# Performance work log

Measured on AMD Instinct MI355X. Metric: run time of the kernel, lower is better.

## Reference

```python
import jax, jax.numpy as jnp
import numpy as np

B, NQ, HW, D, H = 4, 100, 4096, 1024, 16
HD = D // H  # head dim = 64
EPS = 1e-5
NEG = -1e9


def layernorm(x, g, b):
    mu = jnp.mean(x, axis=-1, keepdims=True)
    var = jnp.mean(jnp.square(x - mu), axis=-1, keepdims=True)
    return (x - mu) * jax.lax.rsqrt(var + EPS) * g + b


def setup_inputs() -> dict:
    key = jax.random.key(0)
    ks = jax.random.split(key, 6)
    scale = 0.02
    return {
        "q": jax.random.normal(ks[0], (B, NQ, D), dtype=jnp.float32),
        "kv": jax.random.normal(ks[1], (B, HW, D), dtype=jnp.float32),
        "mask": jax.random.randint(ks[2], (B, NQ, HW), 0, 2, dtype=jnp.int32),
        "in_proj_w": scale * jax.random.normal(ks[3], (3 * D, D), dtype=jnp.float32),
        "in_proj_b": jnp.zeros((3 * D,), dtype=jnp.float32),
        "out_w": scale * jax.random.normal(ks[4], (D, D), dtype=jnp.float32),
        "out_b": jnp.zeros((D,), dtype=jnp.float32),
        "g_q": jnp.ones((D,), dtype=jnp.float32),
        "b_q": jnp.zeros((D,), dtype=jnp.float32),
        "g_kv": jnp.ones((D,), dtype=jnp.float32),
        "b_kv": jnp.zeros((D,), dtype=jnp.float32),
    }


def reference(q, kv, mask, in_proj_w, in_proj_b, out_w, out_b, g_q, b_q, g_kv, b_kv):
    qn = layernorm(q, g_q, b_q)      # [B,NQ,D]
    kvn = layernorm(kv, g_kv, b_kv)  # [B,HW,D]

    # nn.MultiheadAttention fused in-projection: rows [Wq; Wk; Wv]
    Wq, Wk, Wv = jnp.split(in_proj_w, 3, axis=0)
    bq, bk, bv = jnp.split(in_proj_b, 3, axis=0)
    qp = (qn @ Wq.T + bq).reshape(B, NQ, H, HD)
    kp = (kvn @ Wk.T + bk).reshape(B, HW, H, HD)
    vp = (kvn @ Wv.T + bv).reshape(B, HW, H, HD)

    scores = jnp.einsum("bqhd,bkhd->bhqk", qp, kp) / jnp.sqrt(jnp.float32(HD))

    # Per-query key mask; a query with an all-zero mask attends everywhere
    # (original code sets key_padding_mask=None when kpm.all()).
    allowed = mask.astype(bool)                                   # [B,NQ,HW]
    has_any = jnp.any(allowed, axis=-1, keepdims=True)
    eff = jnp.where(has_any, allowed, True)
    scores = jnp.where(eff[:, None, :, :], scores, NEG)

    attn = jax.nn.softmax(scores, axis=-1)                        # [B,H,NQ,HW]
    ctx = jnp.einsum("bhqk,bkhd->bqhd", attn, vp).reshape(B, NQ, D)
    return ctx @ out_w.T + out_b
```

## Files before the change

kernel.cpp:

```cpp
#include <hip/hip_runtime.h>
#include <math.h>
#include <stdint.h>

#define B_    4
#define NQ_   100
#define HW_   4096
#define D_    1024
#define H_    16
#define HD_   64
#define NCH_  8
#define KCH_  (HW_/NCH_)
#define QT_   32
#define MP_   512

typedef __attribute__((ext_vector_type(8))) short short8;
typedef __attribute__((ext_vector_type(8))) unsigned short ushort8v;
typedef __attribute__((ext_vector_type(4))) float f32x4;

__device__ __forceinline__ unsigned short f2bf(float f) {
    unsigned int u = __float_as_uint(f);
    u += 0x7fffu + ((u >> 16) & 1u);
    return (unsigned short)(u >> 16);
}
__device__ __forceinline__ float bf2f(unsigned short h) {
    return __uint_as_float(((unsigned int)h) << 16);
}

__device__ __forceinline__ void gl2lds16(const void* g, void* l) {
    typedef __attribute__((address_space(1))) unsigned int gu32;
    typedef __attribute__((address_space(3))) unsigned int lu32;
    __builtin_amdgcn_global_load_lds(
        reinterpret_cast<gu32*>(reinterpret_cast<uintptr_t>(g)),
        reinterpret_cast<lu32*>(reinterpret_cast<uintptr_t>(l)),
        16, 0, 0);
}

__global__ __launch_bounds__(256) void ln_bf16_kernel(
    const float* __restrict__ x, const float* __restrict__ g,
    const float* __restrict__ be, unsigned short* __restrict__ y, int real_rows)
{
    const int wv = threadIdx.x >> 6, lane = threadIdx.x & 63;
    const int row = blockIdx.x * 4 + wv;
    unsigned short* yr = y + (size_t)row * D_;
    if (row >= real_rows) {
        #pragma unroll
        for (int k = 0; k < 4; ++k)
            *reinterpret_cast<ushort4*>(yr + lane*4 + k*256) = make_ushort4(0,0,0,0);
        return;
    }
    const float* xr = x + (size_t)row * D_;
    float4 v[4];
    float s = 0.f, ss = 0.f;
    #pragma unroll
    for (int k = 0; k < 4; ++k) {
        v[k] = *reinterpret_cast<const float4*>(xr + lane*4 + k*256);
        s  += v[k].x + v[k].y + v[k].z + v[k].w;
        ss += v[k].x*v[k].x + v[k].y*v[k].y + v[k].z*v[k].z + v[k].w*v[k].w;
    }
    #pragma unroll
    for (int o = 1; o < 64; o <<= 1) {
        s  += __shfl_xor(s,  o);
        ss += __shfl_xor(ss, o);
    }
    const float mu = s * (1.0f / D_);
    const float rs = rsqrtf(ss * (1.0f / D_) - mu*mu + 1e-5f);
    #pragma unroll
    for (int k = 0; k < 4; ++k) {
        const float4 gg = *reinterpret_cast<const float4*>(g  + lane*4 + k*256);
        const float4 bb = *reinterpret_cast<const float4*>(be + lane*4 + k*256);
        ushort4 o;
        o.x = f2bf((v[k].x - mu) * rs * gg.x + bb.x);
        o.y = f2bf((v[k].y - mu) * rs * gg.y + bb.y);
        o.z = f2bf((v[k].z - mu) * rs * gg.z + bb.z);
        o.w = f2bf((v[k].w - mu) * rs * gg.w + bb.w);
        *reinterpret_cast<ushort4*>(yr + lane*4 + k*256) = o;
    }
}

__global__ __launch_bounds__(256) void wconv_kernel(
    const float* __restrict__ w, unsigned short* __restrict__ wb)
{
    const int i = blockIdx.x * 256 + threadIdx.x;
    const float4 v = reinterpret_cast<const float4*>(w)[i];
    ushort4 o;
    o.x = f2bf(v.x); o.y = f2bf(v.y); o.z = f2bf(v.z); o.w = f2bf(v.w);
    reinterpret_cast<ushort4*>(wb)[i] = o;
}

__global__ __launch_bounds__(256) void hilo_a_kernel(
    const float* __restrict__ x, unsigned short* __restrict__ y)
{
    const int row = blockIdx.x;
    const int tid = threadIdx.x;
    unsigned short* yr = y + (size_t)row * 3072;
    if (row >= B_*NQ_) {
        const ushort4 z = make_ushort4(0,0,0,0);
        reinterpret_cast<ushort4*>(yr)[tid]        = z;
        reinterpret_cast<ushort4*>(yr + 1024)[tid] = z;
        reinterpret_cast<ushort4*>(yr + 2048)[tid] = z;
        return;
    }
    const float4 v = reinterpret_cast<const float4*>(x + (size_t)row * D_)[tid];
    ushort4 hi, lo;
    hi.x = f2bf(v.x); hi.y = f2bf(v.y); hi.z = f2bf(v.z); hi.w = f2bf(v.w);
    lo.x = f2bf(v.x - bf2f(hi.x)); lo.y = f2bf(v.y - bf2f(hi.y));
    lo.z = f2bf(v.z - bf2f(hi.z)); lo.w = f2bf(v.w - bf2f(hi.w));
    reinterpret_cast<ushort4*>(yr)[tid]        = hi;
    reinterpret_cast<ushort4*>(yr + 1024)[tid] = lo;
    reinterpret_cast<ushort4*>(yr + 2048)[tid] = hi;
}

__global__ __launch_bounds__(256) void hilo_w_kernel(
    const float* __restrict__ w, unsigned short* __restrict__ y)
{
    const int row = blockIdx.x;
    const int tid = threadIdx.x;
    const float4 v = reinterpret_cast<const float4*>(w + (size_t)row * D_)[tid];
    ushort4 hi, lo;
    hi.x = f2bf(v.x); hi.y = f2bf(v.y); hi.z = f2bf(v.z); hi.w = f2bf(v.w);
    lo.x = f2bf(v.x - bf2f(hi.x)); lo.y = f2bf(v.y - bf2f(hi.y));
    lo.z = f2bf(v.z - bf2f(hi.z)); lo.w = f2bf(v.w - bf2f(hi.w));
    unsigned short* yr = y + (size_t)row * 3072;
    reinterpret_cast<ushort4*>(yr)[tid]        = hi;
    reinterpret_cast<ushort4*>(yr + 1024)[tid] = hi;
    reinterpret_cast<ushort4*>(yr + 2048)[tid] = lo;
}

__global__ __launch_bounds__(256) void mpack_kernel(
    const int* __restrict__ mask, unsigned int* __restrict__ mp)
{
    const int qrow = blockIdx.x;
    const int b = blockIdx.y;
    const int tid = threadIdx.x;
    unsigned int word = 0;
    if (qrow < NQ_ && tid < 128) {
        const int4* mr = reinterpret_cast<const int4*>(
            mask + ((size_t)(b*NQ_ + qrow))*HW_ + tid*32);
        #pragma unroll
        for (int j = 0; j < 8; ++j) {
            const int4 v = mr[j];
            word |= (v.x!=0 ? 1u:0u) << (4*j);
            word |= (v.y!=0 ? 1u:0u) << (4*j+1);
            word |= (v.z!=0 ? 1u:0u) << (4*j+2);
            word |= (v.w!=0 ? 1u:0u) << (4*j+3);
        }
    }
    const int wany = __any(word != 0) ? 1 : 0;
    __shared__ int red[4];
    if ((tid & 63) == 0) red[tid >> 6] = wany;
    __syncthreads();
    const int hasany = red[0] | red[1] | red[2] | red[3];
    if (tid < 128)
        mp[((size_t)(b*128 + qrow))*128 + tid] = hasany ? word : 0xFFFFFFFFu;
}

__global__ __launch_bounds__(256) void gemm_kv_kernel(
    const unsigned short* __restrict__ A, const unsigned short* __restrict__ Wb,
    const float* __restrict__ bias, unsigned short* __restrict__ kp,
    unsigned short* __restrict__ vt)
{
    const int K = D_;
    __shared__ __align__(16) unsigned short As[4096];
    __shared__ __align__(16) unsigned short Bs[4096];

    const int tid  = threadIdx.x;
    const int wave = tid >> 6, lane = tid & 63;
    const int bn = blockIdx.x, bm = blockIdx.y;
    const int wm = (wave >> 1) * 64, wn = (wave & 1) * 64;

    const int r0  = tid >> 2;
    const int xs  = (r0 & 3) ^ ((r0 >> 2) & 3);
    const int kc  = (tid & 3) ^ xs;
    const unsigned short* ap0 = A  + (size_t)(bm*128 + r0      )*K + kc*8;
    const unsigned short* ap1 = A  + (size_t)(bm*128 + r0 + 64 )*K + kc*8;
    const unsigned short* bp0 = Wb + (size_t)(bn*128 + r0      )*K + kc*8;
    const unsigned short* bp1 = Wb + (size_t)(bn*128 + r0 + 64 )*K + kc*8;
    unsigned short* asd0 = As + wave*512;
    unsigned short* asd1 = As + 2048 + wave*512;
    unsigned short* bsd0 = Bs + wave*512;
    unsigned short* bsd1 = Bs + 2048 + wave*512;

    f32x4 acc[4][4];
    #pragma unroll
    for (int i = 0; i < 4; ++i)
        #pragma unroll
        for (int j = 0; j < 4; ++j)
            acc[i][j] = (f32x4){0.f, 0.f, 0.f, 0.f};

    const int lr = lane & 15, lq = lane >> 4;
    const int xl = (lr & 3) ^ ((lr >> 2) & 3);
    const int qs = (lq ^ xl) * 8;

    for (int kb = 0; kb < K; kb += 32) {
        gl2lds16(ap0, asd0); gl2lds16(ap1, asd1);
        gl2lds16(bp0, bsd0); gl2lds16(bp1, bsd1);
        ap0 += 32; ap1 += 32; bp0 += 32; bp1 += 32;
        __syncthreads();
        short8 af[4], bf[4];
        #pragma unroll
        for (int i = 0; i < 4; ++i) {
            af[i] = *reinterpret_cast<const short8*>(&As[(wm + i*16 + lr)*32 + qs]);
            bf[i] = *reinterpret_cast<const short8*>(&Bs[(wn + i*16 + lr)*32 + qs]);
        }
        #pragma unroll
        for (int i = 0; i < 4; ++i)
            #pragma unroll
            for (int j = 0; j < 4; ++j)
                acc[i][j] = __builtin_amdgcn_mfma_f32_16x16x32_bf16(
                    af[i], bf[j], acc[i][j], 0, 0, 0);
        __syncthreads();
    }

    const int row0 = bm*128 + wm + lq*4;
    const int col0 = bn*128 + wn + lr;
    if (bn < 8) {
        #pragma unroll
        for (int j = 0; j < 4; ++j) {
            const int n = col0 + j*16;
            const float bb = bias[n];
            #pragma unroll
            for (int i = 0; i < 4; ++i) {
                unsigned short* Cp = kp + (size_t)(row0 + i*16) * 1024 + n;
                #pragma unroll
                for (int r = 0; r < 4; ++r)
                    Cp[(size_t)r * 1024] = f2bf(acc[i][j][r] + bb);
            }
        }
    } else {
        const int b = bm >> 5;
        const int key0base = row0 - b*4096;
        #pragma unroll
        for (int j = 0; j < 4; ++j) {
            const int n = col0 + j*16;
            const float bb = bias[n];
            unsigned short* vrow = vt + (size_t)(b*1024 + n - 1024) * HW_;
            #pragma unroll
            for (int i = 0; i < 4; ++i) {
                ushort4 o;
                o.x = f2bf(acc[i][j][0] + bb);
                o.y = f2bf(acc[i][j][1] + bb);
                o.z = f2bf(acc[i][j][2] + bb);
                o.w = f2bf(acc[i][j][3] + bb);
                *reinterpret_cast<ushort4*>(vrow + key0base + i*16) = o;
            }
        }
    }
}

__global__ __launch_bounds__(256) void gemm_splitk_kernel(
    const unsigned short* __restrict__ A, const unsigned short* __restrict__ W,
    float* __restrict__ P, int K, int KS)
{
    __shared__ __align__(16) unsigned short As[2048];
    __shared__ __align__(16) unsigned short Bs[2048];
    const int tid = threadIdx.x;
    const int wave = tid >> 6, lane = tid & 63;
    const int lr = lane & 15, quad = lane >> 4;
    const int bn = blockIdx.x, bm = blockIdx.y, sk = blockIdx.z;

    const int r0 = tid >> 2;
    const int xs = (r0 & 3) ^ ((r0 >> 2) & 3);
    const int kc = (tid & 3) ^ xs;
    const unsigned short* ap = A + (size_t)(bm*64 + r0)*K + sk*KS + kc*8;
    const unsigned short* bp = W + (size_t)(bn*64 + r0)*K + sk*KS + kc*8;
    unsigned short* asd = As + wave*512;
    unsigned short* bsd = Bs + wave*512;

    f32x4 acc[4];
    #pragma unroll
    for (int j = 0; j < 4; ++j) acc[j] = (f32x4){0.f,0.f,0.f,0.f};

    const int arow = wave*16 + lr;
    const int xa = (arow & 3) ^ ((arow >> 2) & 3);
    const int aoff = (arow*4 + (quad ^ xa))*8;
    int boff[4];
    #pragma unroll
    for (int j = 0; j < 4; ++j) {
        const int brow = j*16 + lr;
        const int xb = (brow & 3) ^ ((brow >> 2) & 3);
        boff[j] = (brow*4 + (quad ^ xb))*8;
    }

    const int nsteps = KS >> 5;
    for (int s = 0; s < nsteps; ++s) {
        gl2lds16(ap, asd); gl2lds16(bp, bsd);
        ap += 32; bp += 32;
        __syncthreads();
        const short8 af = *reinterpret_cast<const short8*>(&As[aoff]);
        short8 bf[4];
        #pragma unroll
        for (int j = 0; j < 4; ++j)
            bf[j] = *reinterpret_cast<const short8*>(&Bs[boff[j]]);
        #pragma unroll
        for (int j = 0; j < 4; ++j)
            acc[j] = __builtin_amdgcn_mfma_f32_16x16x32_bf16(af, bf[j], acc[j], 0, 0, 0);
        __syncthreads();
    }

    float* Pb = P + ((size_t)sk*MP_ + bm*64)*1024 + bn*64;
    const int m0 = wave*16 + quad*4;
    #pragma unroll
    for (int j = 0; j < 4; ++j)
        #pragma unroll
        for (int r = 0; r < 4; ++r)
            Pb[(size_t)(m0 + r)*1024 + j*16 + lr] = acc[j][r];
}

__global__ __launch_bounds__(256) void reduce_kernel(
    const float* __restrict__ P, const float* __restrict__ bias,
    float* __restrict__ Cout, int SK)
{
    const int i4 = blockIdx.x * 256 + threadIdx.x;
    const int c4 = i4 & 255;
    float4 s = reinterpret_cast<const float4*>(bias)[c4];
    for (int sk = 0; sk < SK; ++sk) {
        const float4 p = reinterpret_cast<const float4*>(P + (size_t)sk*MP_*1024)[i4];
        s.x += p.x; s.y += p.y; s.z += p.z; s.w += p.w;
    }
    reinterpret_cast<float4*>(Cout)[i4] = s;
}

__global__ __launch_bounds__(256) void flash_kernel(
    const float* __restrict__ qp, const unsigned short* __restrict__ kp,
    const unsigned short* __restrict__ vt, const unsigned int* __restrict__ mpack,
    float* __restrict__ partO, float* __restrict__ partL)
{
    __shared__ __align__(16) unsigned char smem[49152];
    unsigned short* Ks  = (unsigned short*)smem;
    unsigned short* Vts = (unsigned short*)(smem + 16384);
    unsigned short* Qs  = (unsigned short*)(smem + 32768);
    unsigned short* Ps  = (unsigned short*)(smem + 37376);
    unsigned int*   MWs = (unsigned int*)  (smem + 47616);
    float*          mlW = (float*)         (smem + 48128);
    float*          Om  = (float*)smem;

    const int tid = threadIdx.x;
    const int wave = tid >> 6, lane = tid & 63;
    const int lr = lane & 15, quad = lane >> 4;
    const int qt = blockIdx.x, h = blockIdx.y;
    const int b = blockIdx.z >> 3, ks = blockIdx.z & 7;
    const int kb0 = ks * KCH_;

    {
        const int q = tid >> 3, dc = (tid & 7) * 8;
        const int qg = qt*QT_ + q;
        float4 v0 = make_float4(0.f,0.f,0.f,0.f), v1 = v0;
        if (qg < NQ_) {
            const float* src = qp + ((size_t)(b*NQ_ + qg))*D_ + h*HD_ + dc;
            v0 = *reinterpret_cast<const float4*>(src);
            v1 = *reinterpret_cast<const float4*>(src + 4);
        }
        ushort8v o;
        o[0]=f2bf(v0.x*0.125f); o[1]=f2bf(v0.y*0.125f);
        o[2]=f2bf(v0.z*0.125f); o[3]=f2bf(v0.w*0.125f);
        o[4]=f2bf(v1.x*0.125f); o[5]=f2bf(v1.y*0.125f);
        o[6]=f2bf(v1.z*0.125f); o[7]=f2bf(v1.w*0.125f);
        *reinterpret_cast<ushort8v*>(&Qs[q*72 + dc]) = o;
    }

    const unsigned short* kptr[4];
    const unsigned short* vptr[4];
    #pragma unroll
    for (int i = 0; i < 4; ++i) {
        const int s = i*256 + tid;
        const int key = s >> 3, jg = (s & 7) ^ (key & 7);
        kptr[i] = kp + ((size_t)(b*HW_) + kb0 + key)*1024 + h*HD_ + jg*8;
        const int d = s >> 4, js = s & 15, jg2 = js ^ (d & 15);
        vptr[i] = vt + ((size_t)(b*1024 + h*HD_ + d))*HW_ + kb0 + jg2*8;
    }

    int koff[2][2], voff[4];
    #pragma unroll
    for (int kj = 0; kj < 2; ++kj)
        #pragma unroll
        for (int ds = 0; ds < 2; ++ds) {
            const int key_l = wave*32 + kj*16 + lr;
            const int jg = ds*4 + quad;
            koff[kj][ds] = (key_l*8 + (jg ^ (key_l & 7))) * 8;
        }
    #pragma unroll
    for (int dj = 0; dj < 4; ++dj) {
        const int d_l = dj*16 + lr;
        const int jg = wave*4 + quad;
        voff[dj] = (d_l*16 + (jg ^ (d_l & 15))) * 8;
    }

    float lreg[8];
    #pragma unroll
    for (int i = 0; i < 8; ++i) lreg[i] = 0.f;
    f32x4 Ov[2][4];
    #pragma unroll
    for (int i = 0; i < 2; ++i)
        #pragma unroll
        for (int j = 0; j < 4; ++j)
            Ov[i][j] = (f32x4){0.f,0.f,0.f,0.f};

    for (int kt = 0; kt < 4; ++kt) {
        __syncthreads();
        #pragma unroll
        for (int i = 0; i < 4; ++i) {
            gl2lds16(kptr[i], Ks  + (i*256 + wave*64)*8);
            gl2lds16(vptr[i], Vts + (i*256 + wave*64)*8);
            kptr[i] += 128*1024; vptr[i] += 128;
        }
        if (tid < 128) {
            const int mw = tid >> 5, mq = tid & 31;
            MWs[mw*32 + mq] = mpack[((size_t)(b*128 + qt*QT_ + mq))*128 +
                                    (ks*16 + kt*4 + mw)];
        }
        __syncthreads();

        f32x4 S[2][2];
        #pragma unroll
        for (int i = 0; i < 2; ++i)
            #pragma unroll
            for (int kj = 0; kj < 2; ++kj)
                S[i][kj] = (f32x4){0.f,0.f,0.f,0.f};
        #pragma unroll
        for (int ds = 0; ds < 2; ++ds) {
            short8 aq[2], bk[2];
            aq[0] = *reinterpret_cast<const short8*>(&Qs[(     lr)*72 + ds*32 + quad*8]);
            aq[1] = *reinterpret_cast<const short8*>(&Qs[(16 + lr)*72 + ds*32 + quad*8]);
            bk[0] = *reinterpret_cast<const short8*>(&Ks[koff[0][ds]]);
            bk[1] = *reinterpret_cast<const short8*>(&Ks[koff[1][ds]]);
            #pragma unroll
            for (int i = 0; i < 2; ++i)
                #pragma unroll
                for (int kj = 0; kj < 2; ++kj)
                    S[i][kj] = __builtin_amdgcn_mfma_f32_16x16x32_bf16(
                        aq[i], bk[kj], S[i][kj], 0, 0, 0);
        }

        #pragma unroll
        for (int i = 0; i < 2; ++i) {
            #pragma unroll
            for (int r = 0; r < 4; ++r) {
                const int q = i*16 + quad*4 + r;
                const unsigned int mw = MWs[wave*32 + q];
                const float p0 = ((mw >> lr) & 1u)        ? __expf(S[i][0][r]) : 0.f;
                const float p1 = ((mw >> (16 + lr)) & 1u) ? __expf(S[i][1][r]) : 0.f;
                lreg[i*4+r] += p0 + p1;
                const float p0n = __shfl_xor(p0, 1);
                const float p1n = __shfl_xor(p1, 1);
                if (!(lr & 1)) {
                    const unsigned int w0 = (unsigned)f2bf(p0) | ((unsigned)f2bf(p0n) << 16);
                    const unsigned int w1 = (unsigned)f2bf(p1) | ((unsigned)f2bf(p1n) << 16);
                    *reinterpret_cast<unsigned int*>(&Ps[wave*1280 + q*40 + lr])      = w0;
                    *reinterpret_cast<unsigned int*>(&Ps[wave*1280 + q*40 + 16 + lr]) = w1;
                }
            }
        }

        short8 pf[2], vf[4];
        #pragma unroll
        for (int i = 0; i < 2; ++i)
            pf[i] = *reinterpret_cast<const short8*>(&Ps[wave*1280 + (i*16+lr)*40 + quad*8]);
        #pragma unroll
        for (int dj = 0; dj < 4; ++dj)
            vf[dj] = *reinterpret_cast<const short8*>(&Vts[voff[dj]]);
        #pragma unroll
        for (int i = 0; i < 2; ++i)
            #pragma unroll
            for (int dj = 0; dj < 4; ++dj)
                Ov[i][dj] = __builtin_amdgcn_mfma_f32_16x16x32_bf16(
                    pf[i], vf[dj], Ov[i][dj], 0, 0, 0);
    }

    __syncthreads();
    #pragma unroll
    for (int i = 0; i < 2; ++i)
        #pragma unroll
        for (int r = 0; r < 4; ++r) {
            float l = lreg[i*4+r];
            #pragma unroll
            for (int o = 1; o < 16; o <<= 1) l += __shfl_xor(l, o);
            if (lr == 0) mlW[wave*32 + i*16 + quad*4 + r] = l;
        }
    #pragma unroll
    for (int i = 0; i < 2; ++i)
        #pragma unroll
        for (int dj = 0; dj < 4; ++dj)
            #pragma unroll
            for (int r = 0; r < 4; ++r) {
                const int q = i*16 + quad*4 + r;
                Om[wave*2112 + q*66 + dj*16 + lr] = Ov[i][dj][r];
            }
    __syncthreads();
    {
        const int q = tid >> 3, dc = (tid & 7) * 8;
        float L = 0.f;
        #pragma unroll
        for (int w = 0; w < 4; ++w) L += mlW[w*32 + q];
        float os[8] = {};
        #pragma unroll
        for (int w = 0; w < 4; ++w)
            #pragma unroll
            for (int j = 0; j < 8; ++j)
                os[j] += Om[w*2112 + q*66 + dc + j];
        const size_t pr = (((size_t)(b*H_ + h))*NCH_ + ks)*128 + qt*QT_ + q;
        *reinterpret_cast<float4*>(&partO[pr*HD_ + dc])     = make_float4(os[0],os[1],os[2],os[3]);
        *reinterpret_cast<float4*>(&partO[pr*HD_ + dc + 4]) = make_float4(os[4],os[5],os[6],os[7]);
        if ((tid & 7) == 0) partL[pr] = L;
    }
}

__global__ __launch_bounds__(64) void combine_kernel(
    const float* __restrict__ partO, const float* __restrict__ partL,
    float* __restrict__ ctx)
{
    const int d = threadIdx.x;
    const int qi = blockIdx.x, h = blockIdx.y, b = blockIdx.z;
    const size_t base = ((size_t)(b*H_ + h)) * NCH_ * 128;
    float L = 0.f, O = 0.f;
    #pragma unroll
    for (int i = 0; i < NCH_; ++i) {
        const size_t r = base + i*128 + qi;
        L += partL[r];
        O += partO[r*HD_ + d];
    }
    ctx[((size_t)(b*NQ_ + qi))*D_ + h*HD_ + d] = O / L;
}

extern "C" void kernel_launch(void* const* d_in, const int* in_sizes, int n_in,
                              void* d_out, int out_size, void* d_ws, size_t ws_size,
                              hipStream_t stream)
{
    const float* q     = (const float*)d_in[0];
    const float* kv    = (const float*)d_in[1];
    const int*   mask  = (const int*)  d_in[2];
    const float* in_w  = (const float*)d_in[3];
    const float* in_b  = (const float*)d_in[4];
    const float* out_w = (const float*)d_in[5];
    const float* out_b = (const float*)d_in[6];
    const float* g_q   = (const float*)d_in[7];
    const float* b_q   = (const float*)d_in[8];
    const float* g_kv  = (const float*)d_in[9];
    const float* b_kv  = (const float*)d_in[10];
    float* out = (float*)d_out;

    char* ws = (char*)d_ws;
    float*          qp       = (float*)         (ws + 0);
    unsigned int*   mpackp   = (unsigned int*)  (ws + 1638400);
    unsigned short* wfull_bf = (unsigned short*)(ws + 1900544);
    unsigned short* qn_bf    = (unsigned short*)(ws + 8192000);
    unsigned short* ctx_cat  = (unsigned short*)(ws + 9240576);
    unsigned short* wout_cat = (unsigned short*)(ws + 12386304);
    float*          P        = (float*)         (ws + 18677760);
    float*          ctx      = (float*)         (ws + 35454976);
    float*          partL    = (float*)         (ws + 37093376);
    float*          partO    = (float*)         (ws + 37355520);
    unsigned short* kvn_bf   = (unsigned short*)(ws + 54132736);
    unsigned short* kp       = (unsigned short*)(ws + 87687168);
    unsigned short* vt       = (unsigned short*)(ws + 121241600);

    mpack_kernel<<<dim3(128, B_), 256, 0, stream>>>(mask, mpackp);
    wconv_kernel<<<3*D_*D_/4/256, 256, 0, stream>>>(in_w, wfull_bf);
    ln_bf16_kernel<<<B_*HW_/4, 256, 0, stream>>>(kv, g_kv, b_kv, kvn_bf, B_*HW_);
    ln_bf16_kernel<<<MP_/4, 256, 0, stream>>>(q, g_q, b_q, qn_bf, B_*NQ_);

    gemm_splitk_kernel<<<dim3(D_/64, MP_/64, 8), 256, 0, stream>>>(
        qn_bf, wfull_bf, P, D_, 128);
    reduce_kernel<<<B_*NQ_*D_/4/256, 256, 0, stream>>>(P, in_b, qp, 8);

    gemm_kv_kernel<<<dim3(16, B_*HW_/128), 256, 0, stream>>>(
        kvn_bf, wfull_bf + (size_t)D_*D_, in_b + D_, kp, vt);

    flash_kernel<<<dim3(4, H_, B_*NCH_), 256, 0, stream>>>(
        qp, kp, vt, mpackp, partO, partL);
    combine_kernel<<<dim3(NQ_, H_, B_), 64, 0, stream>>>(partO, partL, ctx);

    hilo_a_kernel<<<MP_, 256, 0, stream>>>(ctx, ctx_cat);
    hilo_w_kernel<<<D_, 256, 0, stream>>>(out_w, wout_cat);
    gemm_splitk_kernel<<<dim3(D_/64, MP_/64, 8), 256, 0, stream>>>(
        ctx_cat, wout_cat, P, 3*D_, 384);
    reduce_kernel<<<B_*NQ_*D_/4/256, 256, 0, stream>>>(P, out_b, out, 8);
}
```

Baseline: 332.8 us.

## Rewrite KV projection GEMM with 256x256 tiles and 4-stage LDS pipeline

The K/V projection GEMM moves from 128x128 tiles with 256 threads and a single-buffered LDS stage to 256x256 tiles with 512 threads (8 waves, each computing a 128x64 sub-tile). Global-to-LDS loads now run through a 4-deep ring buffer using explicit vmcnt waits, barriers and raised MFMA priority, so memory traffic overlaps compute. The larger tile raises operand reuse per byte loaded. In exchange the kernel uses 128KB of dynamic LDS and many more accumulator registers, the launch grid is smaller, and the waitcnt/barrier sequencing is fragile.

Result: no change. 327.1 us (-1.7%).

```diff
diff --git a/kernel.cpp b/kernel.cpp
--- a/kernel.cpp
+++ b/kernel.cpp
@@ -34,6 +34,11 @@
         reinterpret_cast<lu32*>(reinterpret_cast<uintptr_t>(l)),
         16, 0, 0);
 }
+
+#define VMCNT8() asm volatile("s_waitcnt vmcnt(8)" ::: "memory")
+#define VMCNT0() asm volatile("s_waitcnt vmcnt(0)" ::: "memory")
+#define BARRIER() do { __builtin_amdgcn_s_barrier(); \
+                       __builtin_amdgcn_sched_barrier(0); } while (0)
 
 __global__ __launch_bounds__(256) void ln_bf16_kernel(
     const float* __restrict__ x, const float* __restrict__ g,
@@ -154,94 +159,137 @@
         mp[((size_t)(b*128 + qrow))*128 + tid] = hasany ? word : 0xFFFFFFFFu;
 }
 
-__global__ __launch_bounds__(256) void gemm_kv_kernel(
+__global__ __launch_bounds__(512, 2) void gemm_kv_kernel(
     const unsigned short* __restrict__ A, const unsigned short* __restrict__ Wb,
     const float* __restrict__ bias, unsigned short* __restrict__ kp,
     unsigned short* __restrict__ vt)
 {
-    const int K = D_;
-    __shared__ __align__(16) unsigned short As[4096];
-    __shared__ __align__(16) unsigned short Bs[4096];
+    extern __shared__ __align__(16) unsigned short lds[];
+    unsigned short* As = lds;
+    unsigned short* Bs = lds + 32768;
 
     const int tid  = threadIdx.x;
-    const int wave = tid >> 6, lane = tid & 63;
-    const int bn = blockIdx.x, bm = blockIdx.y;
-    const int wm = (wave >> 1) * 64, wn = (wave & 1) * 64;
-
-    const int r0  = tid >> 2;
-    const int xs  = (r0 & 3) ^ ((r0 >> 2) & 3);
-    const int kc  = (tid & 3) ^ xs;
-    const unsigned short* ap0 = A  + (size_t)(bm*128 + r0      )*K + kc*8;
-    const unsigned short* ap1 = A  + (size_t)(bm*128 + r0 + 64 )*K + kc*8;
-    const unsigned short* bp0 = Wb + (size_t)(bn*128 + r0      )*K + kc*8;
-    const unsigned short* bp1 = Wb + (size_t)(bn*128 + r0 + 64 )*K + kc*8;
-    unsigned short* asd0 = As + wave*512;
-    unsigned short* asd1 = As + 2048 + wave*512;
-    unsigned short* bsd0 = Bs + wave*512;
-    unsigned short* bsd1 = Bs + 2048 + wave*512;
-
-    f32x4 acc[4][4];
-    #pragma unroll
-    for (int i = 0; i < 4; ++i)
+    const int wave = tid >> 6;
+    const int lane = tid & 63;
+    const int lr   = lane & 15, quad = lane >> 4;
+    const int wm2  = wave >> 2;
+    const int wn4  = wave & 3;
+
+    const int bn = blockIdx.x & 7;
+    const int bm = blockIdx.x >> 3;
+
+    const int swz_src = ((lane >> 2) & 3) ^ (lane >> 4);
+    const int scol    = ((lane & 3) ^ swz_src) * 8;
+    const unsigned short* aSrc0 = A  + (size_t)(bm*256 +       wave*16 + (lane>>2))*D_ + scol;
+    const unsigned short* aSrc1 = A  + (size_t)(bm*256 + 128 + wave*16 + (lane>>2))*D_ + scol;
+    const unsigned short* bSrc0 = Wb + (size_t)(bn*256 +       wave*16 + (lane>>2))*D_ + scol;
+    const unsigned short* bSrc1 = Wb + (size_t)(bn*256 + 128 + wave*16 + (lane>>2))*D_ + scol;
+    const int wdst = wave * 512;
+
+    const int kq = (quad ^ (lr & 3) ^ (lr >> 2)) * 8;
+    int aoff[8], boff[4];
+    #pragma unroll
+    for (int fm = 0; fm < 8; ++fm) aoff[fm] = (wm2*128 + fm*16 + lr)*32 + kq;
+    #pragma unroll
+    for (int fn = 0; fn < 4; ++fn) boff[fn] = (wn4*64  + fn*16 + lr)*32 + kq;
+
+    f32x4 acc[8][4];
+    #pragma unroll
+    for (int i = 0; i < 8; ++i)
         #pragma unroll
         for (int j = 0; j < 4; ++j)
             acc[i][j] = (f32x4){0.f, 0.f, 0.f, 0.f};
 
-    const int lr = lane & 15, lq = lane >> 4;
-    const int xl = (lr & 3) ^ ((lr >> 2) & 3);
-    const int qs = (lq ^ xl) * 8;
-
-    for (int kb = 0; kb < K; kb += 32) {
-        gl2lds16(ap0, asd0); gl2lds16(ap1, asd1);
-        gl2lds16(bp0, bsd0); gl2lds16(bp1, bsd1);
-        ap0 += 32; ap1 += 32; bp0 += 32; bp1 += 32;
-        __syncthreads();
-        short8 af[4], bf[4];
-        #pragma unroll
-        for (int i = 0; i < 4; ++i) {
-            af[i] = *reinterpret_cast<const short8*>(&As[(wm + i*16 + lr)*32 + qs]);
-            bf[i] = *reinterpret_cast<const short8*>(&Bs[(wn + i*16 + lr)*32 + qs]);
-        }
-        #pragma unroll
-        for (int i = 0; i < 4; ++i)
-            #pragma unroll
-            for (int j = 0; j < 4; ++j)
-                acc[i][j] = __builtin_amdgcn_mfma_f32_16x16x32_bf16(
-                    af[i], bf[j], acc[i][j], 0, 0, 0);
-        __syncthreads();
-    }
-
-    const int row0 = bm*128 + wm + lq*4;
-    const int col0 = bn*128 + wn + lr;
-    if (bn < 8) {
-        #pragma unroll
-        for (int j = 0; j < 4; ++j) {
-            const int n = col0 + j*16;
+    #pragma unroll
+    for (int pt = 0; pt < 3; ++pt) {
+        gl2lds16(aSrc0 + pt*32, As + pt*8192 + wdst);
+        gl2lds16(aSrc1 + pt*32, As + pt*8192 + 4096 + wdst);
+        gl2lds16(bSrc0 + pt*32, Bs + pt*8192 + wdst);
+        gl2lds16(bSrc1 + pt*32, Bs + pt*8192 + 4096 + wdst);
+    }
+    VMCNT8();
+    BARRIER();
+
+    #pragma unroll 1
+    for (int t = 0; t < 32; ++t) {
+        const unsigned short* Asl = As + (t & 3) * 8192;
+        const unsigned short* Bsl = Bs + (t & 3) * 8192;
+        const int s3 = (t + 3) & 3;
+        short8 afr[4], bfr[4];
+
+        #pragma unroll
+        for (int fm = 0; fm < 4; ++fm)
+            afr[fm] = *reinterpret_cast<const short8*>(&Asl[aoff[fm]]);
+        #pragma unroll
+        for (int fn = 0; fn < 4; ++fn)
+            bfr[fn] = *reinterpret_cast<const short8*>(&Bsl[boff[fn]]);
+        if (t < 29) {
+            gl2lds16(aSrc0 + (t+3)*32, As + s3*8192 + wdst);
+            gl2lds16(aSrc1 + (t+3)*32, As + s3*8192 + 4096 + wdst);
+        }
+        BARRIER();
+        __builtin_amdgcn_s_setprio(1);
+        #pragma unroll
+        for (int fm = 0; fm < 4; ++fm)
+            #pragma unroll
+            for (int fn = 0; fn < 4; ++fn)
+                acc[fm][fn] = __builtin_amdgcn_mfma_f32_16x16x32_bf16(
+                    afr[fm], bfr[fn], acc[fm][fn], 0, 0, 0);
+        __builtin_amdgcn_s_setprio(0);
+        BARRIER();
+
+        #pragma unroll
+        for (int fm = 0; fm < 4; ++fm)
+            afr[fm] = *reinterpret_cast<const short8*>(&Asl[aoff[fm + 4]]);
+        if (t < 29) {
+            gl2lds16(bSrc0 + (t+3)*32, Bs + s3*8192 + wdst);
+            gl2lds16(bSrc1 + (t+3)*32, Bs + s3*8192 + 4096 + wdst);
+        }
+        BARRIER();
+        __builtin_amdgcn_s_setprio(1);
+        #pragma unroll
+        for (int fm = 0; fm < 4; ++fm)
+            #pragma unroll
+            for (int fn = 0; fn < 4; ++fn)
+                acc[fm + 4][fn] = __builtin_amdgcn_mfma_f32_16x16x32_bf16(
+                    afr[fm], bfr[fn], acc[fm + 4][fn], 0, 0, 0);
+        __builtin_amdgcn_s_setprio(0);
+        if (t < 29)      { VMCNT8(); }
+        else if (t < 31) { VMCNT0(); }
+        BARRIER();
+    }
+
+    const int colbase = bn*256 + wn4*64 + lr;
+    const int mbase   = bm*256 + wm2*128 + quad*4;
+    if (bn < 4) {
+        #pragma unroll
+        for (int fn = 0; fn < 4; ++fn) {
+            const int n = colbase + fn*16;
             const float bb = bias[n];
             #pragma unroll
-            for (int i = 0; i < 4; ++i) {
-                unsigned short* Cp = kp + (size_t)(row0 + i*16) * 1024 + n;
+            for (int fm = 0; fm < 8; ++fm) {
+                unsigned short* Cp = kp + (size_t)(mbase + fm*16)*1024 + n;
                 #pragma unroll
                 for (int r = 0; r < 4; ++r)
-                    Cp[(size_t)r * 1024] = f2bf(acc[i][j][r] + bb);
+                    Cp[(size_t)r * 1024] = f2bf(acc[fm][fn][r] + bb);
             }
         }
     } else {
-        const int b = bm >> 5;
-        const int key0base = row0 - b*4096;
-        #pragma unroll
-        for (int j = 0; j < 4; ++j) {
-            const int n = col0 + j*16;
+        const int b = bm >> 4;
+        const int key0 = mbase - b*4096;
+        #pragma unroll
+        for (int fn = 0; fn < 4; ++fn) {
+            const int n = colbase + fn*16;
             const float bb = bias[n];
             unsigned short* vrow = vt + (size_t)(b*1024 + n - 1024) * HW_;
             #pragma unroll
-            for (int i = 0; i < 4; ++i) {
+            for (int fm = 0; fm < 8; ++fm) {
                 ushort4 o;
-                o.x = f2bf(acc[i][j][0] + bb);
-                o.y = f2bf(acc[i][j][1] + bb);
-                o.z = f2bf(acc[i][j][2] + bb);
-                o.w = f2bf(acc[i][j][3] + bb);
-                *reinterpret_cast<ushort4*>(vrow + key0base + i*16) = o;
+                o.x = f2bf(acc[fm][fn][0] + bb);
+                o.y = f2bf(acc[fm][fn][1] + bb);
+                o.z = f2bf(acc[fm][fn][2] + bb);
+                o.w = f2bf(acc[fm][fn][3] + bb);
+                *reinterpret_cast<ushort4*>(vrow + key0 + fm*16) = o;
             }
         }
     }
@@ -553,6 +601,13 @@
     unsigned short* kp       = (unsigned short*)(ws + 87687168);
     unsigned short* vt       = (unsigned short*)(ws + 121241600);
 
+    static bool attr_set = false;
+    if (!attr_set) {
+        hipFuncSetAttribute(reinterpret_cast<const void*>(gemm_kv_kernel),
+                            hipFuncAttributeMaxDynamicSharedMemorySize, 131072);
+        attr_set = true;
+    }
+
     mpack_kernel<<<dim3(128, B_), 256, 0, stream>>>(mask, mpackp);
     wconv_kernel<<<3*D_*D_/4/256, 256, 0, stream>>>(in_w, wfull_bf);
     ln_bf16_kernel<<<B_*HW_/4, 256, 0, stream>>>(kv, g_kv, b_kv, kvn_bf, B_*HW_);
@@ -562,7 +617,7 @@
         qn_bf, wfull_bf, P, D_, 128);
     reduce_kernel<<<B_*NQ_*D_/4/256, 256, 0, stream>>>(P, in_b, qp, 8);
 
-    gemm_kv_kernel<<<dim3(16, B_*HW_/128), 256, 0, stream>>>(
+    gemm_kv_kernel<<<512, 512, 131072, stream>>>(
         kvn_bf, wfull_bf + (size_t)D_*D_, in_b + D_, kp, vt);
 
     flash_kernel<<<dim3(4, H_, B_*NCH_), 256, 0, stream>>>(
```
